# Kernel tuning notes

Hardware: AMD Instinct MI355X
Metric: run time of the kernel (lower is better)

Reference implementation:

```python
import jax, jax.numpy as jnp
import numpy as np

N_NODES = 100000
N_EDGES = 1600000
IN_CH = 128
HIDDEN = 128
OUT_CH = 64


def _glorot(key, shape):
    fan_in, fan_out = shape
    lim = jnp.sqrt(6.0 / (fan_in + fan_out))
    return jax.random.uniform(key, shape, jnp.float32, -lim, lim)


def setup_inputs() -> dict:
    key = jax.random.key(0)
    ks = jax.random.split(key, 8)
    x = jax.random.normal(ks[0], (N_NODES, IN_CH), jnp.float32)
    edge_index = jax.random.randint(ks[1], (2, N_EDGES), 0, N_NODES, jnp.int64)
    return {
        "x": x,
        "edge_index": edge_index,
        "W1": _glorot(ks[2], (IN_CH, HIDDEN)),
        "b1": jnp.zeros((HIDDEN,), jnp.float32),
        "W2": _glorot(ks[3], (HIDDEN, HIDDEN)),
        "b2": jnp.zeros((HIDDEN,), jnp.float32),
        "W3": _glorot(ks[4], (HIDDEN, HIDDEN)),
        "b3": jnp.zeros((HIDDEN,), jnp.float32),
        "Wout": _glorot(ks[5], (HIDDEN, OUT_CH)),
        "bout": jnp.zeros((OUT_CH,), jnp.float32),
    }


def _gcn_conv(h, W, b, src, dst, norm, num_nodes):
    # h: [N, F_in] -> linear transform first (PyG GCNConv order)
    h = h @ W                                   # [N, F_out]
    msg = h[src] * norm[:, None]                # [E+N, F_out] gathered+scaled
    agg = jax.ops.segment_sum(msg, dst, num_segments=num_nodes)
    return agg + b


def reference(x, edge_index, W1, b1, W2, b2, W3, b3, Wout, bout):
    n = x.shape[0]
    # add self-loops (PyG GCNConv default)
    loop = jnp.arange(n, dtype=edge_index.dtype)
    src = jnp.concatenate([edge_index[0], loop])
    dst = jnp.concatenate([edge_index[1], loop])
    # symmetric normalization: deg^-1/2[src] * deg^-1/2[dst]
    deg = jax.ops.segment_sum(jnp.ones_like(dst, dtype=x.dtype), dst, num_segments=n)
    inv_sqrt = jnp.where(deg > 0, jax.lax.rsqrt(deg), 0.0)
    norm = inv_sqrt[src] * inv_sqrt[dst]        # [E+N]

    h = jax.nn.relu(_gcn_conv(x, W1, b1, src, dst, norm, n))
    # dropout p=0.2 is identity in eval mode
    h = jax.nn.relu(_gcn_conv(h, W2, b2, src, dst, norm, n))
    h = _gcn_conv(h, W3, b3, src, dst, norm, n)
    return h @ Wout + bout                      # [N, OUT_CH]
```

## Files before the change

### kernel.cpp

```cpp
#include <hip/hip_runtime.h>

typedef unsigned int uint;
typedef _Float16 half_t;
typedef __attribute__((ext_vector_type(8))) _Float16 halfx8;
typedef __attribute__((ext_vector_type(4))) float floatx4;
typedef __attribute__((ext_vector_type(4))) uint uintx4;

constexpr int BSHIFT  = 9;
constexpr int BNODES  = 1 << BSHIFT;
constexpr int BCAP    = 9216;
constexpr int CSTRIDE = 16;
constexpr int CHUNK   = 8192;

__device__ __forceinline__ void fmix_lo(float& a, uint h2, float w) {
    asm("v_fma_mix_f32 %0, %1, %2, %0 op_sel:[0,0,0] op_sel_hi:[1,0,0]"
        : "+v"(a) : "v"(h2), "v"(w));
}
__device__ __forceinline__ void fmix_hi(float& a, uint h2, float w) {
    asm("v_fma_mix_f32 %0, %1, %2, %0 op_sel:[1,0,0] op_sel_hi:[1,0,0]"
        : "+v"(a) : "v"(h2), "v"(w));
}

__device__ __forceinline__ halfx8 gload16(const half_t* p) {
    halfx8 r;
    asm volatile("global_load_dwordx4 %0, %1, off" : "=v"(r) : "v"(p));
    return r;
}

__global__ __launch_bounds__(256) void k_mega0(
    const int* __restrict__ ei,
    const float* __restrict__ W1, const float* __restrict__ W2,
    const float* __restrict__ W3, const float* __restrict__ Wout,
    const float* __restrict__ b3, const float* __restrict__ bout,
    int* __restrict__ bcnt, uint* __restrict__ tmp,
    half_t* __restrict__ Wh1, half_t* __restrict__ Wh2,
    half_t* __restrict__ Whc, float* __restrict__ bc,
    int E, int nSort) {
    __shared__ __align__(16) char smem[45088];
    const int bx = blockIdx.x, t = threadIdx.x;

    if (bx < nSort) {
        uint* ent = (uint*)smem;
        unsigned char* bid = (unsigned char*)(smem + 32768);
        int* hist  = (int*)(smem + 40960);
        int* lbase = hist + 256;
        int* lcur  = hist + 512;
        int* gpos  = hist + 768;
        int* wsum  = hist + 1024;
        const int base = bx * CHUNK;
        const int m = min(CHUNK, E - base);
        hist[t] = 0;
        __syncthreads();
        for (int i = t; i < m; i += 256)
            atomicAdd(&hist[ei[E + base + i] >> BSHIFT], 1);
        __syncthreads();
        {
            int lane = t & 63, w = t >> 6;
            int v = hist[t];
            int incl = v;
            for (int dd = 1; dd < 64; dd <<= 1) { int xsh = __shfl_up(incl, dd); if (lane >= dd) incl += xsh; }
            if (lane == 63) wsum[w] = incl;
            __syncthreads();
            int off = 0;
            for (int i = 0; i < w; i++) off += wsum[i];
            int excl = off + incl - v;
            lbase[t] = excl;
            lcur[t]  = excl;
            gpos[t]  = (v > 0) ? atomicAdd(&bcnt[t * CSTRIDE], v) : 0;
        }
        __syncthreads();
        for (int i = t; i < m; i += 256) {
            int s = ei[base + i];
            int d = ei[E + base + i];
            int b = d >> BSHIFT;
            int pos = atomicAdd(&lcur[b], 1);
            ent[pos] = (uint)s | ((uint)(d & (BNODES - 1)) << 17);
            bid[pos] = (unsigned char)b;
        }
        __syncthreads();
        for (int i = t; i < m; i += 256) {
            int b = bid[i];
            int g = gpos[b] + (i - lbase[b]);
            if (g < BCAP) tmp[(size_t)b * BCAP + g] = ent[i];
        }
    } else if (bx < nSort + 64) {
        int i = (bx - nSort) * 256 + t;
        int k = i >> 7, n = i & 127;
        Wh1[n * 128 + k] = (half_t)W1[k * 128 + n];
    } else if (bx < nSort + 128) {
        int i = (bx - nSort - 64) * 256 + t;
        int k = i >> 7, n = i & 127;
        Wh2[n * 128 + k] = (half_t)W2[k * 128 + n];
    } else {
        int i = (bx - nSort - 128) * 256 + t;
        if (i < 128 * 64) {
            int r = i >> 6, j = i & 63;
            float s = 0.0f;
            for (int k = 0; k < 128; k++) s += W3[r * 128 + k] * Wout[k * 64 + j];
            Whc[j * 128 + r] = (half_t)s;
        } else if (i < 128 * 64 + 64) {
            int j = i - 128 * 64;
            float s = bout[j];
            for (int k = 0; k < 128; k++) s += b3[k] * Wout[k * 64 + j];
            bc[j] = s;
        }
    }
}

__global__ __launch_bounds__(256) void k_mid(
    const uint* __restrict__ tmp, const int* __restrict__ bcnt,
    float* __restrict__ inv, int* __restrict__ bbase,
    int* __restrict__ row_ptr, int N, int B) {
    __shared__ int cnt[BNODES];
    int bx = blockIdx.x, t = threadIdx.x;
    if (bx < B) {
        cnt[t] = 0; cnt[t + 256] = 0;
        __syncthreads();
        int m = min(bcnt[bx * CSTRIDE], BCAP);
        const uint* tp = tmp + (size_t)bx * BCAP;
        for (int i = t; i < m; i += 256) atomicAdd(&cnt[tp[i] >> 17], 1);
        __syncthreads();
        int nbase = bx << BSHIFT;
        int n0 = nbase + t, n1 = nbase + t + 256;
        if (n0 < N) inv[n0] = rsqrtf((float)(cnt[t] + 1));
        if (n1 < N) inv[n1] = rsqrtf((float)(cnt[t + 256] + 1));
    } else {
        int* wsum = cnt;
        int lane = t & 63, w = t >> 6;
        int v = (t < B) ? min(bcnt[t * CSTRIDE], BCAP) : 0;
        int incl = v;
        for (int d = 1; d < 64; d <<= 1) { int x = __shfl_up(incl, d); if (lane >= d) incl += x; }
        if (lane == 63) wsum[w] = incl;
        __syncthreads();
        int off = 0;
        for (int i = 0; i < w; i++) off += wsum[i];
        int excl = off + incl - v;
        if (t <= B) bbase[t] = excl;
        if (t == B) row_ptr[N] = excl;
    }
}

__global__ __launch_bounds__(256) void k_mega1(
    const float* __restrict__ A, const half_t* __restrict__ Wh,
    const float* __restrict__ inv, half_t* __restrict__ Out,
    const uint* __restrict__ tmp, const int* __restrict__ bcnt,
    const int* __restrict__ bbase, int* __restrict__ row_ptr,
    int* __restrict__ colv, int N, int nGemm) {
    __shared__ __align__(16) char smem1[128 * 136 * 2];
    const int bx = blockIdx.x, tid = threadIdx.x;

    if (bx >= nGemm) {
        int* cnt = (int*)smem1;
        int* cur = cnt + BNODES;
        int* wsum2 = cur + BNODES;
        int b = bx - nGemm, t = tid;
        int base = bbase[b], nbase = b << BSHIFT;
        cnt[t] = 0; cnt[t + 256] = 0;
        __syncthreads();
        int m = min(bcnt[b * CSTRIDE], BCAP);
        const uint* tp = tmp + (size_t)b * BCAP;
        for (int i = t; i < m; i += 256) atomicAdd(&cnt[tp[i] >> 17], 1);
        __syncthreads();
        int lane = t & 63, w = t >> 6;
        int c0 = cnt[2 * t], c1 = cnt[2 * t + 1];
        int v = c0 + c1;
        int incl = v;
        for (int dd = 1; dd < 64; dd <<= 1) { int x = __shfl_up(incl, dd); if (lane >= dd) incl += x; }
        if (lane == 63) wsum2[w] = incl;
        __syncthreads();
        int off = 0;
        for (int i = 0; i < w; i++) off += wsum2[i];
        int excl = off + incl - v;
        int n0 = nbase + 2 * t, n1 = nbase + 2 * t + 1;
        __syncthreads();
        cur[2 * t] = excl; cur[2 * t + 1] = excl + c0;
        if (n0 < N) row_ptr[n0] = base + excl;
        if (n1 < N) row_ptr[n1] = base + excl + c0;
        __syncthreads();
        for (int i = t; i < m; i += 256) {
            uint wv = tp[i];
            int dlo = wv >> 17, s = (int)(wv & 0x1FFFFu);
            int pos = atomicAdd(&cur[dlo], 1);
            colv[base + pos] = s;
        }
        return;
    }
    half_t* lds = (half_t*)smem1;
    for (int i = tid; i < 128 * 16; i += 256) {
        int r = i >> 4, c = i & 15;
        *(halfx8*)&lds[r * 136 + c * 8] = *(const halfx8*)&Wh[(size_t)r * 128 + c * 8];
    }
    __syncthreads();
    const int w = tid >> 6, lane = tid & 63;
    const int q = lane >> 4, m = lane & 15;
    const int rowBase = bx * 128 + w * 32;
    int arow[2];
#pragma unroll
    for (int rt = 0; rt < 2; ++rt) {
        int r = rowBase + rt * 16 + m;
        arow[rt] = (r < N) ? r : (N - 1);
    }
    floatx4 acc[2][8];
#pragma unroll
    for (int rt = 0; rt < 2; ++rt)
#pragma unroll
        for (int ct = 0; ct < 8; ++ct) acc[rt][ct] = (floatx4)0.0f;
#pragma unroll
    for (int kk = 0; kk < 4; ++kk) {
        halfx8 a[2];
#pragma unroll
        for (int rt = 0; rt < 2; ++rt) {
            const float* ap = A + (size_t)arow[rt] * 128 + kk * 32 + q * 8;
            floatx4 f0 = *(const floatx4*)ap;
            floatx4 f1 = *(const floatx4*)(ap + 4);
#pragma unroll
            for (int i = 0; i < 4; i++) { a[rt][i] = (half_t)f0[i]; a[rt][4 + i] = (half_t)f1[i]; }
        }
#pragma unroll
        for (int ct = 0; ct < 8; ++ct) {
            halfx8 bh = *(const halfx8*)&lds[(ct * 16 + m) * 136 + kk * 32 + q * 8];
#pragma unroll
            for (int rt = 0; rt < 2; ++rt)
                acc[rt][ct] = __builtin_amdgcn_mfma_f32_16x16x32_f16(a[rt], bh, acc[rt][ct], 0, 0, 0);
        }
    }
#pragma unroll
    for (int rt = 0; rt < 2; ++rt)
#pragma unroll
        for (int r = 0; r < 4; ++r) {
            int orow = rowBase + rt * 16 + q * 4 + r;
            if (orow < N) {
                float sc = inv[orow];
#pragma unroll
                for (int ct = 0; ct < 8; ++ct)
                    Out[(size_t)orow * 128 + ct * 16 + m] = (half_t)(sc * acc[rt][ct][r]);
            }
        }
}

template <int NOUT>
__global__ __launch_bounds__(256) void k_gemm(const half_t* __restrict__ A,
                                              const half_t* __restrict__ Wh,
                                              const float* __restrict__ inv,
                                              half_t* __restrict__ Out, int nRows) {
    constexpr int CT = NOUT / 16;
    __shared__ __align__(16) half_t lds[NOUT * 136];
    const int tid = threadIdx.x;
    for (int i = tid; i < NOUT * 16; i += 256) {
        int r = i >> 4, c = i & 15;
        *(halfx8*)&lds[r * 136 + c * 8] = *(const halfx8*)&Wh[(size_t)r * 128 + c * 8];
    }
    __syncthreads();
    const int w = tid >> 6, lane = tid & 63;
    const int q = lane >> 4, m = lane & 15;
    const int rowBase = blockIdx.x * 128 + w * 32;
    int arow[2];
#pragma unroll
    for (int rt = 0; rt < 2; ++rt) {
        int r = rowBase + rt * 16 + m;
        arow[rt] = (r < nRows) ? r : (nRows - 1);
    }
    floatx4 acc[2][CT];
#pragma unroll
    for (int rt = 0; rt < 2; ++rt)
#pragma unroll
        for (int ct = 0; ct < CT; ++ct) acc[rt][ct] = (floatx4)0.0f;
#pragma unroll
    for (int kk = 0; kk < 4; ++kk) {
        halfx8 a[2];
#pragma unroll
        for (int rt = 0; rt < 2; ++rt)
            a[rt] = *(const halfx8*)(A + (size_t)arow[rt] * 128 + kk * 32 + q * 8);
#pragma unroll
        for (int ct = 0; ct < CT; ++ct) {
            halfx8 bh = *(const halfx8*)&lds[(ct * 16 + m) * 136 + kk * 32 + q * 8];
#pragma unroll
            for (int rt = 0; rt < 2; ++rt)
                acc[rt][ct] = __builtin_amdgcn_mfma_f32_16x16x32_f16(a[rt], bh, acc[rt][ct], 0, 0, 0);
        }
    }
#pragma unroll
    for (int rt = 0; rt < 2; ++rt)
#pragma unroll
        for (int r = 0; r < 4; ++r) {
            int orow = rowBase + rt * 16 + q * 4 + r;
            if (orow < nRows) {
                float sc = inv[orow];
#pragma unroll
                for (int ct = 0; ct < CT; ++ct)
                    Out[(size_t)orow * NOUT + ct * 16 + m] = (half_t)(sc * acc[rt][ct][r]);
            }
        }
}

template <int CH, typename OT, bool RELU>
__global__ __launch_bounds__(256) void k_agg(const half_t* __restrict__ tb,
                                             const int* __restrict__ colv,
                                             const int* __restrict__ row_ptr,
                                             const float* __restrict__ inv,
                                             const float* __restrict__ bias,
                                             OT* __restrict__ out, int N) {
    constexpr int L = CH / 8;
    constexpr int G = 64 / L;
    int wid = threadIdx.x >> 6, lane = threadIdx.x & 63;
    int d = blockIdx.x * 4 + wid;
    if (d >= N) return;
    int beg = row_ptr[d], end = row_ptr[d + 1];
    int grp = lane / L;
    int choff = (lane % L) * 8;
    const float one = 1.0f;
    const half_t* tbc = tb + choff;

    halfx8 pself = *(const halfx8*)(tbc + (size_t)d * CH);
    float isd = inv[d];

    float af[8];
#pragma unroll
    for (int c = 0; c < 8; c++) af[c] = 0.0f;

    for (int e0 = beg; e0 < end; e0 += 64) {
        int me = e0 + lane;
        int sl = 0; float wl = 0.0f;
        if (me < end) { sl = colv[me]; wl = 1.0f; }
        int cnt = end - e0; if (cnt > 64) cnt = 64;
        int j = 0;
        for (; j + 4 * G <= cnt; j += 4 * G) {
            int s4[4];
#pragma unroll
            for (int u = 0; u < 4; u++) s4[u] = __shfl(sl, j + u * G + grp);
            halfx8 pv[4];
#pragma unroll
            for (int u = 0; u < 4; u++)
                pv[u] = gload16(tbc + (size_t)s4[u] * CH);
            asm volatile("s_waitcnt vmcnt(0)" ::: "memory");
            __builtin_amdgcn_sched_barrier(0);
#pragma unroll
            for (int u = 0; u < 4; u++) {
                uintx4 pw = __builtin_bit_cast(uintx4, pv[u]);
#pragma unroll
                for (int c = 0; c < 8; c++) {
                    if (c & 1) fmix_hi(af[c], pw[c >> 1], one);
                    else       fmix_lo(af[c], pw[c >> 1], one);
                }
            }
        }
        if (j < cnt) {
            int s4[4]; float w4[4];
#pragma unroll
            for (int u = 0; u < 4; u++) {
                int idx = j + u * G + grp;
                s4[u] = __shfl(sl, idx);
                w4[u] = __shfl(wl, idx);
            }
            halfx8 pv[4];
#pragma unroll
            for (int u = 0; u < 4; u++)
                pv[u] = gload16(tbc + (size_t)s4[u] * CH);
            asm volatile("s_waitcnt vmcnt(0)" ::: "memory");
            __builtin_amdgcn_sched_barrier(0);
#pragma unroll
            for (int u = 0; u < 4; u++) {
                uintx4 pw = __builtin_bit_cast(uintx4, pv[u]);
#pragma unroll
                for (int c = 0; c < 8; c++) {
                    if (c & 1) fmix_hi(af[c], pw[c >> 1], w4[u]);
                    else       fmix_lo(af[c], pw[c >> 1], w4[u]);
                }
            }
        }
    }
    {
        float ws0 = (grp == 0) ? 1.0f : 0.0f;
        uintx4 pw = __builtin_bit_cast(uintx4, pself);
#pragma unroll
        for (int c = 0; c < 8; c++) {
            if (c & 1) fmix_hi(af[c], pw[c >> 1], ws0);
            else       fmix_lo(af[c], pw[c >> 1], ws0);
        }
    }
#pragma unroll
    for (int msk = L; msk < 64; msk <<= 1)
#pragma unroll
        for (int c = 0; c < 8; c++)
            af[c] += __shfl_xor(af[c], msk);

    if (lane < L) {
        int ch = lane * 8;
        floatx4 b0 = *(const floatx4*)(bias + ch);
        floatx4 b1 = *(const floatx4*)(bias + ch + 4);
#pragma unroll
        for (int c = 0; c < 8; c++) {
            af[c] = isd * af[c] + ((c < 4) ? b0[c] : b1[c - 4]);
            if (RELU) af[c] = fmaxf(af[c], 0.0f);
        }
        if constexpr (sizeof(OT) == 2) {
            halfx8 o;
#pragma unroll
            for (int c = 0; c < 8; c++) o[c] = (half_t)af[c];
            *(halfx8*)((half_t*)out + (size_t)d * CH + ch) = o;
        } else {
            floatx4 o0, o1;
#pragma unroll
            for (int c = 0; c < 4; c++) { o0[c] = af[c]; o1[c] = af[c + 4]; }
            *(floatx4*)((float*)out + (size_t)d * CH + ch) = o0;
            *(floatx4*)((float*)out + (size_t)d * CH + ch + 4) = o1;
        }
    }
}

extern "C" void kernel_launch(void* const* d_in, const int* in_sizes, int n_in,
                              void* d_out, int out_size, void* d_ws, size_t ws_size,
                              hipStream_t stream) {
    const int N = in_sizes[0] / 128;
    const int E = in_sizes[1] / 2;
    const int B = (N + BNODES - 1) >> BSHIFT;

    const float* x    = (const float*)d_in[0];
    const int*   ei   = (const int*)d_in[1];
    const float* W1   = (const float*)d_in[2];
    const float* b1   = (const float*)d_in[3];
    const float* W2   = (const float*)d_in[4];
    const float* b2   = (const float*)d_in[5];
    const float* W3   = (const float*)d_in[6];
    const float* b3   = (const float*)d_in[7];
    const float* Wout = (const float*)d_in[8];
    const float* bout = (const float*)d_in[9];
    float* out = (float*)d_out;

    char* p = (char*)d_ws;
    auto alloc = [&](size_t bytes) -> void* {
        void* r = (void*)p;
        p += (bytes + 255) & ~(size_t)255;
        return r;
    };
    int*    bcnt    = (int*)alloc((size_t)B * CSTRIDE * 4);
    int*    bbase   = (int*)alloc(((size_t)B + 1) * 4);
    uint*   tmp     = (uint*)alloc((size_t)B * BCAP * 4);
    int*    colv    = (int*)alloc((size_t)E * 4);
    int*    row_ptr = (int*)alloc(((size_t)N + 1) * 4);
    float*  inv     = (float*)alloc((size_t)N * 4);
    float*  bc      = (float*)alloc(64 * 4);
    half_t* Wh1     = (half_t*)alloc(128 * 128 * 2);
    half_t* Wh2     = (half_t*)alloc(128 * 128 * 2);
    half_t* Whc     = (half_t*)alloc(64 * 128 * 2);
    half_t* hb      = (half_t*)alloc((size_t)N * 128 * 2);
    half_t* tb      = (half_t*)alloc((size_t)N * 128 * 2);

    const int nSort = (E + CHUNK - 1) / CHUNK;
    const int nGemm = (N + 127) / 128;
    const int gAgg  = (N + 3) / 4;

    hipMemsetAsync(bcnt, 0, (size_t)B * CSTRIDE * 4, stream);
    k_mega0<<<nSort + 128 + 33, 256, 0, stream>>>(ei, W1, W2, W3, Wout, b3, bout,
                                                  bcnt, tmp, Wh1, Wh2, Whc, bc,
                                                  E, nSort);
    k_mid<<<B + 1, 256, 0, stream>>>(tmp, bcnt, inv, bbase, row_ptr, N, B);
    k_mega1<<<nGemm + B, 256, 0, stream>>>(x, Wh1, inv, tb, tmp, bcnt, bbase,
                                           row_ptr, colv, N, nGemm);
    k_agg<128, half_t, true><<<gAgg, 256, 0, stream>>>(tb, colv, row_ptr, inv, b1, hb, N);
    k_gemm<128><<<nGemm, 256, 0, stream>>>(hb, Wh2, inv, tb, N);
    k_agg<128, half_t, true><<<gAgg, 256, 0, stream>>>(tb, colv, row_ptr, inv, b2, hb, N);
    k_gemm<64><<<nGemm, 256, 0, stream>>>(hb, Whc, inv, tb, N);
    k_agg<64, float, false><<<gAgg, 256, 0, stream>>>(tb, colv, row_ptr, inv, bc, out, N);
}
```

Baseline: 355.5 us.

## Split aggregation channels across blocks to raise parallelism per destination node

The aggregation kernel now splits each node's channel dimension into NQ slices, with each slice handled by a separate block. Each wave therefore covers 32 channels with 4 lanes and 16 edge groups, so one batch of gathers covers all 64 edges in a chunk. The unrolled steady-state loop and the separate tail path are merged into one masked gather step. This adds parallelism and memory-level concurrency, but each gather is now a 16-byte segment instead of a full row. It also repeats the row_ptr and colv reads NQ times per node.

```diff
diff --git a/kernel.cpp b/kernel.cpp
--- a/kernel.cpp
+++ b/kernel.cpp
@@ -293,22 +293,24 @@
         }
 }
 
-template <int CH, typename OT, bool RELU>
+template <int CH, int NQ, typename OT, bool RELU>
 __global__ __launch_bounds__(256) void k_agg(const half_t* __restrict__ tb,
                                              const int* __restrict__ colv,
                                              const int* __restrict__ row_ptr,
                                              const float* __restrict__ inv,
                                              const float* __restrict__ bias,
                                              OT* __restrict__ out, int N) {
-    constexpr int L = CH / 8;
+    constexpr int QCH = CH / NQ;
+    constexpr int L = QCH / 8;
     constexpr int G = 64 / L;
-    int wid = threadIdx.x >> 6, lane = threadIdx.x & 63;
-    int d = blockIdx.x * 4 + wid;
+    const int tid = threadIdx.x;
+    const int wid = tid >> 6, lane = tid & 63;
+    const int c = blockIdx.x % NQ;
+    const int d = (blockIdx.x / NQ) * 4 + wid;
     if (d >= N) return;
-    int beg = row_ptr[d], end = row_ptr[d + 1];
-    int grp = lane / L;
-    int choff = (lane % L) * 8;
-    const float one = 1.0f;
+    const int beg = row_ptr[d], end = row_ptr[d + 1];
+    const int grp = lane / L;
+    const int choff = c * QCH + (lane % L) * 8;
     const half_t* tbc = tb + choff;
 
     halfx8 pself = *(const halfx8*)(tbc + (size_t)d * CH);
@@ -316,55 +318,35 @@
 
     float af[8];
 #pragma unroll
-    for (int c = 0; c < 8; c++) af[c] = 0.0f;
+    for (int ch = 0; ch < 8; ch++) af[ch] = 0.0f;
 
     for (int e0 = beg; e0 < end; e0 += 64) {
         int me = e0 + lane;
         int sl = 0; float wl = 0.0f;
         if (me < end) { sl = colv[me]; wl = 1.0f; }
         int cnt = end - e0; if (cnt > 64) cnt = 64;
-        int j = 0;
-        for (; j + 4 * G <= cnt; j += 4 * G) {
-            int s4[4];
-#pragma unroll
-            for (int u = 0; u < 4; u++) s4[u] = __shfl(sl, j + u * G + grp);
-            halfx8 pv[4];
-#pragma unroll
-            for (int u = 0; u < 4; u++)
+        int nu = (cnt + G - 1) / G;
+        int s4[4]; float w4[4];
+        halfx8 pv[4];
+        static_assert(64 / G <= 4, "");
+#pragma unroll
+        for (int u = 0; u < 64 / G; u++) {
+            if (u < nu) {
+                s4[u] = __shfl(sl, u * G + grp);
+                w4[u] = __shfl(wl, u * G + grp);
                 pv[u] = gload16(tbc + (size_t)s4[u] * CH);
-            asm volatile("s_waitcnt vmcnt(0)" ::: "memory");
-            __builtin_amdgcn_sched_barrier(0);
-#pragma unroll
-            for (int u = 0; u < 4; u++) {
+            }
+        }
+        asm volatile("s_waitcnt vmcnt(0)" ::: "memory");
+        __builtin_amdgcn_sched_barrier(0);
+#pragma unroll
+        for (int u = 0; u < 64 / G; u++) {
+            if (u < nu) {
                 uintx4 pw = __builtin_bit_cast(uintx4, pv[u]);
 #pragma unroll
-                for (int c = 0; c < 8; c++) {
-                    if (c & 1) fmix_hi(af[c], pw[c >> 1], one);
-                    else       fmix_lo(af[c], pw[c >> 1], one);
-                }
-            }
-        }
-        if (j < cnt) {
-            int s4[4]; float w4[4];
-#pragma unroll
-            for (int u = 0; u < 4; u++) {
-                int idx = j + u * G + grp;
-                s4[u] = __shfl(sl, idx);
-                w4[u] = __shfl(wl, idx);
-            }
-            halfx8 pv[4];
-#pragma unroll
-            for (int u = 0; u < 4; u++)
-                pv[u] = gload16(tbc + (size_t)s4[u] * CH);
-            asm volatile("s_waitcnt vmcnt(0)" ::: "memory");
-            __builtin_amdgcn_sched_barrier(0);
-#pragma unroll
-            for (int u = 0; u < 4; u++) {
-                uintx4 pw = __builtin_bit_cast(uintx4, pv[u]);
-#pragma unroll
-                for (int c = 0; c < 8; c++) {
-                    if (c & 1) fmix_hi(af[c], pw[c >> 1], w4[u]);
-                    else       fmix_lo(af[c], pw[c >> 1], w4[u]);
+                for (int ch = 0; ch < 8; ch++) {
+                    if (ch & 1) fmix_hi(af[ch], pw[ch >> 1], w4[u]);
+                    else        fmix_lo(af[ch], pw[ch >> 1], w4[u]);
                 }
             }
         }
@@ -373,37 +355,37 @@
         float ws0 = (grp == 0) ? 1.0f : 0.0f;
         uintx4 pw = __builtin_bit_cast(uintx4, pself);
 #pragma unroll
-        for (int c = 0; c < 8; c++) {
-            if (c & 1) fmix_hi(af[c], pw[c >> 1], ws0);
-            else       fmix_lo(af[c], pw[c >> 1], ws0);
+        for (int ch = 0; ch < 8; ch++) {
+            if (ch & 1) fmix_hi(af[ch], pw[ch >> 1], ws0);
+            else        fmix_lo(af[ch], pw[ch >> 1], ws0);
         }
     }
 #pragma unroll
     for (int msk = L; msk < 64; msk <<= 1)
 #pragma unroll
-        for (int c = 0; c < 8; c++)
-            af[c] += __shfl_xor(af[c], msk);
+        for (int ch = 0; ch < 8; ch++)
+            af[ch] += __shfl_xor(af[ch], msk);
 
     if (lane < L) {
-        int ch = lane * 8;
-        floatx4 b0 = *(const floatx4*)(bias + ch);
-        floatx4 b1 = *(const floatx4*)(bias + ch + 4);
-#pragma unroll
-        for (int c = 0; c < 8; c++) {
-            af[c] = isd * af[c] + ((c < 4) ? b0[c] : b1[c - 4]);
-            if (RELU) af[c] = fmaxf(af[c], 0.0f);
+        int ch0 = c * QCH + lane * 8;
+        floatx4 b0 = *(const floatx4*)(bias + ch0);
+        floatx4 b1 = *(const floatx4*)(bias + ch0 + 4);
+#pragma unroll
+        for (int ch = 0; ch < 8; ch++) {
+            af[ch] = isd * af[ch] + ((ch < 4) ? b0[ch] : b1[ch - 4]);
+            if (RELU) af[ch] = fmaxf(af[ch], 0.0f);
         }
         if constexpr (sizeof(OT) == 2) {
             halfx8 o;
 #pragma unroll
-            for (int c = 0; c < 8; c++) o[c] = (half_t)af[c];
-            *(halfx8*)((half_t*)out + (size_t)d * CH + ch) = o;
+            for (int ch = 0; ch < 8; ch++) o[ch] = (half_t)af[ch];
+            *(halfx8*)((half_t*)out + (size_t)d * CH + ch0) = o;
         } else {
             floatx4 o0, o1;
 #pragma unroll
-            for (int c = 0; c < 4; c++) { o0[c] = af[c]; o1[c] = af[c + 4]; }
-            *(floatx4*)((float*)out + (size_t)d * CH + ch) = o0;
-            *(floatx4*)((float*)out + (size_t)d * CH + ch + 4) = o1;
+            for (int ch = 0; ch < 4; ch++) { o0[ch] = af[ch]; o1[ch] = af[ch + 4]; }
+            *(floatx4*)((float*)out + (size_t)d * CH + ch0) = o0;
+            *(floatx4*)((float*)out + (size_t)d * CH + ch0 + 4) = o1;
         }
     }
 }
@@ -448,7 +430,9 @@
 
     const int nSort = (E + CHUNK - 1) / CHUNK;
     const int nGemm = (N + 127) / 128;
-    const int gAgg  = (N + 3) / 4;
+    const int gRow  = (N + 3) / 4;
+    const int gAgg128 = gRow * 4;
+    const int gAgg64  = gRow * 2;
 
     hipMemsetAsync(bcnt, 0, (size_t)B * CSTRIDE * 4, stream);
     k_mega0<<<nSort + 128 + 33, 256, 0, stream>>>(ei, W1, W2, W3, Wout, b3, bout,
@@ -457,9 +441,9 @@
     k_mid<<<B + 1, 256, 0, stream>>>(tmp, bcnt, inv, bbase, row_ptr, N, B);
     k_mega1<<<nGemm + B, 256, 0, stream>>>(x, Wh1, inv, tb, tmp, bcnt, bbase,
                                            row_ptr, colv, N, nGemm);
-    k_agg<128, half_t, true><<<gAgg, 256, 0, stream>>>(tb, colv, row_ptr, inv, b1, hb, N);
+    k_agg<128, 4, half_t, true><<<gAgg128, 256, 0, stream>>>(tb, colv, row_ptr, inv, b1, hb, N);
     k_gemm<128><<<nGemm, 256, 0, stream>>>(hb, Wh2, inv, tb, N);
-    k_agg<128, half_t, true><<<gAgg, 256, 0, stream>>>(tb, colv, row_ptr, inv, b2, hb, N);
+    k_agg<128, 4, half_t, true><<<gAgg128, 256, 0, stream>>>(tb, colv, row_ptr, inv, b2, hb, N);
     k_gemm<64><<<nGemm, 256, 0, stream>>>(hb, Whc, inv, tb, N);
-    k_agg<64, float, false><<<gAgg, 256, 0, stream>>>(tb, colv, row_ptr, inv, bc, out, N);
-}
+    k_agg<64, 2, float, false><<<gAgg64, 256, 0, stream>>>(tb, colv, row_ptr, inv, bc, out, N);
+}
```

Result: slower. 582.0 us (+63.7%).

## Split 128-channel aggregation into XCD-affine channel halves for L2 locality

Applied to the files above, without the earlier changes.

Replaces the two 128-channel aggregation launches with a kernel that splits features into two 64-channel slices. Blocks read their XCC id from a hardware register and claim work tickets from a per-slice atomic counter, so each XCD group gathers only one half of the feature rows. The aim is to halve the gather working set per L2 and raise cache hit rates on random neighbor reads. The cost is twice the blocks, narrower per-lane loads, atomics at block start, and a fallback path for when one slice's tickets run out.

```diff
diff --git a/kernel.cpp b/kernel.cpp
--- a/kernel.cpp
+++ b/kernel.cpp
@@ -408,6 +408,132 @@
     }
 }
 
+__global__ __launch_bounds__(256) void k_aggs(const half_t* __restrict__ tb,
+                                              const int* __restrict__ colv,
+                                              const int* __restrict__ row_ptr,
+                                              const float* __restrict__ inv,
+                                              const float* __restrict__ bias,
+                                              half_t* __restrict__ out, int N,
+                                              int ntick, int* __restrict__ ctr) {
+    constexpr int CH = 128;
+    constexpr int SW = 64;
+    constexpr int L  = SW / 8;
+    constexpr int G  = 64 / L;
+    const int tid = threadIdx.x;
+    const int wid = tid >> 6, lane = tid & 63;
+
+    __shared__ int tk2[2];
+    if (tid == 0) {
+        uint xcc;
+        asm volatile("s_getreg_b32 %0, hwreg(20, 0, 4)" : "=s"(xcc));
+        int s = (int)(xcc & 1u);
+        int i = atomicAdd(&ctr[s], 1);
+        if (i >= ntick) {
+            s ^= 1;
+            i = atomicAdd(&ctr[s], 1);
+            if (i >= ntick) i = -1;
+        }
+        tk2[0] = i; tk2[1] = s;
+    }
+    __syncthreads();
+    const int tkt = tk2[0];
+    if (tkt < 0) return;
+    const int slc = tk2[1];
+    const int grp = lane / L;
+    const half_t* tbc = tb + slc * SW + (lane % L) * 8;
+    const float one = 1.0f;
+
+    for (int k = 0; k < 4; k++) {
+        int d = tkt * 16 + wid * 4 + k;
+        if (d >= N) return;
+        int beg = row_ptr[d], end = row_ptr[d + 1];
+        halfx8 pself = *(const halfx8*)(tbc + (size_t)d * CH);
+        float isd = inv[d];
+        float af[8];
+#pragma unroll
+        for (int c = 0; c < 8; c++) af[c] = 0.0f;
+
+        for (int e0 = beg; e0 < end; e0 += 64) {
+            int me = e0 + lane;
+            int sv = 0; float wl = 0.0f;
+            if (me < end) { sv = colv[me]; wl = 1.0f; }
+            int cnt = end - e0; if (cnt > 64) cnt = 64;
+            int j = 0;
+            for (; j + 4 * G <= cnt; j += 4 * G) {
+                int s4[4];
+#pragma unroll
+                for (int u = 0; u < 4; u++) s4[u] = __shfl(sv, j + u * G + grp);
+                halfx8 pv[4];
+#pragma unroll
+                for (int u = 0; u < 4; u++)
+                    pv[u] = gload16(tbc + (size_t)s4[u] * CH);
+                asm volatile("s_waitcnt vmcnt(0)" ::: "memory");
+                __builtin_amdgcn_sched_barrier(0);
+#pragma unroll
+                for (int u = 0; u < 4; u++) {
+                    uintx4 pw = __builtin_bit_cast(uintx4, pv[u]);
+#pragma unroll
+                    for (int c = 0; c < 8; c++) {
+                        if (c & 1) fmix_hi(af[c], pw[c >> 1], one);
+                        else       fmix_lo(af[c], pw[c >> 1], one);
+                    }
+                }
+            }
+            if (j < cnt) {
+                int s4[4]; float w4[4];
+#pragma unroll
+                for (int u = 0; u < 4; u++) {
+                    int idx = j + u * G + grp;
+                    s4[u] = __shfl(sv, idx);
+                    w4[u] = __shfl(wl, idx);
+                }
+                halfx8 pv[4];
+#pragma unroll
+                for (int u = 0; u < 4; u++)
+                    pv[u] = gload16(tbc + (size_t)s4[u] * CH);
+                asm volatile("s_waitcnt vmcnt(0)" ::: "memory");
+                __builtin_amdgcn_sched_barrier(0);
+#pragma unroll
+                for (int u = 0; u < 4; u++) {
+                    uintx4 pw = __builtin_bit_cast(uintx4, pv[u]);
+#pragma unroll
+                    for (int c = 0; c < 8; c++) {
+                        if (c & 1) fmix_hi(af[c], pw[c >> 1], w4[u]);
+                        else       fmix_lo(af[c], pw[c >> 1], w4[u]);
+                    }
+                }
+            }
+        }
+        {
+            float ws0 = (grp == 0) ? 1.0f : 0.0f;
+            uintx4 pw = __builtin_bit_cast(uintx4, pself);
+#pragma unroll
+            for (int c = 0; c < 8; c++) {
+                if (c & 1) fmix_hi(af[c], pw[c >> 1], ws0);
+                else       fmix_lo(af[c], pw[c >> 1], ws0);
+            }
+        }
+#pragma unroll
+        for (int msk = L; msk < 64; msk <<= 1)
+#pragma unroll
+            for (int c = 0; c < 8; c++)
+                af[c] += __shfl_xor(af[c], msk);
+
+        if (lane < L) {
+            int ch0 = slc * SW + lane * 8;
+            floatx4 b0 = *(const floatx4*)(bias + ch0);
+            floatx4 b1 = *(const floatx4*)(bias + ch0 + 4);
+            halfx8 o;
+#pragma unroll
+            for (int c = 0; c < 8; c++) {
+                float v = isd * af[c] + ((c < 4) ? b0[c] : b1[c - 4]);
+                o[c] = (half_t)fmaxf(v, 0.0f);
+            }
+            *(halfx8*)(out + (size_t)d * CH + ch0) = o;
+        }
+    }
+}
+
 extern "C" void kernel_launch(void* const* d_in, const int* in_sizes, int n_in,
                               void* d_out, int out_size, void* d_ws, size_t ws_size,
                               hipStream_t stream) {
@@ -435,6 +561,7 @@
     };
     int*    bcnt    = (int*)alloc((size_t)B * CSTRIDE * 4);
     int*    bbase   = (int*)alloc(((size_t)B + 1) * 4);
+    int*    aggctr  = (int*)alloc(4 * 4);
     uint*   tmp     = (uint*)alloc((size_t)B * BCAP * 4);
     int*    colv    = (int*)alloc((size_t)E * 4);
     int*    row_ptr = (int*)alloc(((size_t)N + 1) * 4);
@@ -449,17 +576,21 @@
     const int nSort = (E + CHUNK - 1) / CHUNK;
     const int nGemm = (N + 127) / 128;
     const int gAgg  = (N + 3) / 4;
+    const int ntick = (N + 15) / 16;
 
     hipMemsetAsync(bcnt, 0, (size_t)B * CSTRIDE * 4, stream);
+    hipMemsetAsync(aggctr, 0, 16, stream);
     k_mega0<<<nSort + 128 + 33, 256, 0, stream>>>(ei, W1, W2, W3, Wout, b3, bout,
                                                   bcnt, tmp, Wh1, Wh2, Whc, bc,
                                                   E, nSort);
     k_mid<<<B + 1, 256, 0, stream>>>(tmp, bcnt, inv, bbase, row_ptr, N, B);
     k_mega1<<<nGemm + B, 256, 0, stream>>>(x, Wh1, inv, tb, tmp, bcnt, bbase,
                                            row_ptr, colv, N, nGemm);
-    k_agg<128, half_t, true><<<gAgg, 256, 0, stream>>>(tb, colv, row_ptr, inv, b1, hb, N);
+    k_aggs<<<2 * ntick, 256, 0, stream>>>(tb, colv, row_ptr, inv, b1, hb, N,
+                                          ntick, aggctr);
     k_gemm<128><<<nGemm, 256, 0, stream>>>(hb, Wh2, inv, tb, N);
-    k_agg<128, half_t, true><<<gAgg, 256, 0, stream>>>(tb, colv, row_ptr, inv, b2, hb, N);
+    k_aggs<<<2 * ntick, 256, 0, stream>>>(tb, colv, row_ptr, inv, b2, hb, N,
+                                          ntick, aggctr + 2);
     k_gemm<64><<<nGemm, 256, 0, stream>>>(hb, Whc, inv, tb, N);
     k_agg<64, float, false><<<gAgg, 256, 0, stream>>>(tb, colv, row_ptr, inv, bc, out, N);
 }
```

Result: slower. 568.7 us (+60.0%).
